# Kernel tuning notes

Measured on AMD Instinct MI355X. Metric: run time of the kernel, lower is better.

## Reference

```python
import jax, jax.numpy as jnp
import numpy as np

B, N = 64, 1024


def setup_inputs() -> dict:
    key = jax.random.key(0)
    attns = jax.random.uniform(key, (B, N, N), dtype=jnp.float32)
    return {"attns": attns}


def _diag_means(a):
    # a: [B, n, n]. wave[b, d] = mean_i a[b, i, i+d] over the anti-diagonal offset d = j - i >= 0.
    n = a.shape[-1]
    idx = jnp.arange(n)
    off = idx[None, :] - idx[:, None]            # [n, n], j - i
    mask = off >= 0                              # upper triangle incl. diagonal
    seg = jnp.where(mask, off, 0).reshape(-1)    # lower-tri values are zeroed, so seg 0 is safe
    vals = jnp.where(mask, a, 0.0).reshape(a.shape[0], -1)  # [B, n*n]
    sums = jax.vmap(lambda v: jax.ops.segment_sum(v, seg, num_segments=n))(vals)  # [B, n]
    counts = (n - idx).astype(a.dtype)           # n - d elements on offset-d diagonal
    return sums / counts


def reference(attns):
    waves = _diag_means(attns)                       # [B, N]
    # torch.fft on (real, 0) pairs + L2 norm over (re, im) == FFT magnitude
    spec = jnp.abs(jnp.fft.fft(waves, axis=-1))      # [B, N]
    n = waves.shape[-1]
    sel = spec[:, 1:1 + n // 2]                      # frequencies 1 .. n/2 (exclusive of DC)
    judgement = 1.0 - jnp.max(sel, axis=-1) / jnp.sum(sel, axis=-1)  # peak-ratio per sample
    return jnp.mean(judgement)                       # scalar, mean over batch
```

## Files before the change

kernel.cpp:

```cpp
#include <hip/hip_runtime.h>

#define NN 1024
#define BB 64
#define CHUNKS 32
#define KS 8

#if __has_builtin(__builtin_amdgcn_make_buffer_rsrc) && __has_builtin(__builtin_amdgcn_raw_buffer_load_b128)
#define USE_SRD 1
#else
#define USE_SRD 0
#endif

#if USE_SRD
typedef unsigned int u32x4 __attribute__((ext_vector_type(4)));
static __device__ __forceinline__ float4 srd_load(__amdgpu_buffer_rsrc_t r, int off) {
    u32x4 v = __builtin_amdgcn_raw_buffer_load_b128(r, off, 0, 0);
    float4 f;
    f.x = __uint_as_float(v.x);
    f.y = __uint_as_float(v.y);
    f.z = __uint_as_float(v.z);
    f.w = __uint_as_float(v.w);
    return f;
}
#endif

__global__ __launch_bounds__(256) void diag_partial(const float* __restrict__ attns,
                                                    float* __restrict__ partial) {
    __shared__ float lds[4][1032];
    const int t = blockIdx.x;
    const int b = blockIdx.y;
    const int tid = threadIdx.x;
    const int w = tid >> 6, lane = tid & 63;

    float4 acc0 = make_float4(0.f, 0.f, 0.f, 0.f);
    float4 acc1 = acc0, acc2 = acc0, acc3 = acc0;

    const float* base = attns + (size_t)b * NN * NN;

#if USE_SRD
    const int voff = lane * 16;

#define ROWPAIR(g, srdT, srdB)                                                \
    const int jbT##g = 16 * t + 4 * (g);                                      \
    const int nvT##g = 256 - 4 * t - (g);                                     \
    __amdgpu_buffer_rsrc_t srdT = __builtin_amdgcn_make_buffer_rsrc(          \
        (void*)(base + (size_t)(jbT##g + w) * NN + jbT##g), (short)0,         \
        nvT##g * 16, 0x00020000);                                             \
    const int jbB##g = 1008 - 16 * t + 4 * (g);                               \
    const int nvB##g = 4 + 4 * t - (g);                                       \
    __amdgpu_buffer_rsrc_t srdB = __builtin_amdgcn_make_buffer_rsrc(          \
        (void*)(base + (size_t)(jbB##g + w) * NN + jbB##g), (short)0,         \
        nvB##g * 16, 0x00020000);

    ROWPAIR(0, srdT0, srdB0)
    ROWPAIR(1, srdT1, srdB1)
    ROWPAIR(2, srdT2, srdB2)
    ROWPAIR(3, srdT3, srdB3)
#undef ROWPAIR

#define LOADP(g, srdT, srdB)                                                  \
    float4 xa##g = srd_load(srdT, voff);                                      \
    float4 xb##g = srd_load(srdT, voff + 1024);                               \
    float4 xc##g = srd_load(srdT, voff + 2048);                               \
    float4 xd##g = srd_load(srdT, voff + 3072);                               \
    float4 ya##g = srd_load(srdB, voff);                                      \
    float4 yb##g = srd_load(srdB, voff + 1024);

#define CONSP(g)                                                              \
    {                                                                         \
        if (lane == 0) {                                                      \
            if (w > 0) { xa##g.x = 0.f; ya##g.x = 0.f; }                      \
            if (w > 1) { xa##g.y = 0.f; ya##g.y = 0.f; }                      \
            if (w > 2) { xa##g.z = 0.f; ya##g.z = 0.f; }                      \
        }                                                                     \
        acc0.x += xa##g.x + ya##g.x; acc0.y += xa##g.y + ya##g.y;             \
        acc0.z += xa##g.z + ya##g.z; acc0.w += xa##g.w + ya##g.w;             \
        acc1.x += xb##g.x + yb##g.x; acc1.y += xb##g.y + yb##g.y;             \
        acc1.z += xb##g.z + yb##g.z; acc1.w += xb##g.w + yb##g.w;             \
        acc2.x += xc##g.x; acc2.y += xc##g.y;                                 \
        acc2.z += xc##g.z; acc2.w += xc##g.w;                                 \
        acc3.x += xd##g.x; acc3.y += xd##g.y;                                 \
        acc3.z += xd##g.z; acc3.w += xd##g.w;                                 \
    }

    LOADP(0, srdT0, srdB0)
    LOADP(1, srdT1, srdB1)
    LOADP(2, srdT2, srdB2)
    CONSP(0)
    LOADP(3, srdT3, srdB3)
    CONSP(1)
    CONSP(2)
    CONSP(3)
#undef LOADP
#undef CONSP

#else

#define ROWPAIR(k, fT, fB, nvT, nvB)                                          \
    const int jbT##k = 16 * t + 4 * (k);                                      \
    const int nvT = 256 - 4 * t - (k);                                        \
    const float4* fT = (const float4*)(base + (size_t)(jbT##k + w) * NN + jbT##k); \
    const int jbB##k = 1008 - 16 * t + 4 * (k);                               \
    const int nvB = 4 + 4 * t - (k);                                          \
    const float4* fB = (const float4*)(base + (size_t)(jbB##k + w) * NN + jbB##k);

    ROWPAIR(0, fT0, fB0, nvT0, nvB0)
    ROWPAIR(1, fT1, fB1, nvT1, nvB1)
    ROWPAIR(2, fT2, fB2, nvT2, nvB2)
    ROWPAIR(3, fT3, fB3, nvT3, nvB3)
#undef ROWPAIR

#define LOADP(g, fT, fB, nvT, nvB)                                            \
    float4 xa##g = fT[lane];                                                  \
    float4 xb##g = fT[lane + 64];                                             \
    float4 xc##g = fT[lane + 128 < nvT - 1 ? lane + 128 : nvT - 1];           \
    float4 xd##g = fT[lane + 192 < nvT - 1 ? lane + 192 : nvT - 1];           \
    float4 ya##g = fB[lane < nvB - 1 ? lane : nvB - 1];                       \
    float4 yb##g = fB[lane + 64 < nvB - 1 ? lane + 64 : nvB - 1];

#define CONSP(g, nvT, nvB)                                                    \
    {                                                                         \
        const bool ok2 = lane + 128 < nvT, ok3 = lane + 192 < nvT;            \
        const bool p0 = lane < nvB, p1 = lane + 64 < nvB;                     \
        xc##g.x = ok2 ? xc##g.x : 0.f; xc##g.y = ok2 ? xc##g.y : 0.f;         \
        xc##g.z = ok2 ? xc##g.z : 0.f; xc##g.w = ok2 ? xc##g.w : 0.f;         \
        xd##g.x = ok3 ? xd##g.x : 0.f; xd##g.y = ok3 ? xd##g.y : 0.f;         \
        xd##g.z = ok3 ? xd##g.z : 0.f; xd##g.w = ok3 ? xd##g.w : 0.f;         \
        ya##g.x = p0 ? ya##g.x : 0.f; ya##g.y = p0 ? ya##g.y : 0.f;           \
        ya##g.z = p0 ? ya##g.z : 0.f; ya##g.w = p0 ? ya##g.w : 0.f;           \
        yb##g.x = p1 ? yb##g.x : 0.f; yb##g.y = p1 ? yb##g.y : 0.f;           \
        yb##g.z = p1 ? yb##g.z : 0.f; yb##g.w = p1 ? yb##g.w : 0.f;           \
        if (lane == 0) {                                                      \
            if (w > 0) { xa##g.x = 0.f; ya##g.x = 0.f; }                      \
            if (w > 1) { xa##g.y = 0.f; ya##g.y = 0.f; }                      \
            if (w > 2) { xa##g.z = 0.f; ya##g.z = 0.f; }                      \
        }                                                                     \
        acc0.x += xa##g.x + ya##g.x; acc0.y += xa##g.y + ya##g.y;             \
        acc0.z += xa##g.z + ya##g.z; acc0.w += xa##g.w + ya##g.w;             \
        acc1.x += xb##g.x + yb##g.x; acc1.y += xb##g.y + yb##g.y;             \
        acc1.z += xb##g.z + yb##g.z; acc1.w += xb##g.w + yb##g.w;             \
        acc2.x += xc##g.x; acc2.y += xc##g.y;                                 \
        acc2.z += xc##g.z; acc2.w += xc##g.w;                                 \
        acc3.x += xd##g.x; acc3.y += xd##g.y;                                 \
        acc3.z += xd##g.z; acc3.w += xd##g.w;                                 \
    }

    LOADP(0, fT0, fB0, nvT0, nvB0)
    LOADP(1, fT1, fB1, nvT1, nvB1)
    LOADP(2, fT2, fB2, nvT2, nvB2)
    CONSP(0, nvT0, nvB0)
    LOADP(3, fT3, fB3, nvT3, nvB3)
    CONSP(1, nvT1, nvB1)
    CONSP(2, nvT2, nvB2)
    CONSP(3, nvT3, nvB3)
#undef LOADP
#undef CONSP
#endif

    float4* lrow = (float4*)lds[w];
    lrow[lane]       = acc0;
    lrow[lane + 64]  = acc1;
    lrow[lane + 128] = acc2;
    lrow[lane + 192] = acc3;
    if (tid < 32) lds[tid >> 3][1024 + (tid & 7)] = 0.f;
    __syncthreads();

    float* outp = partial + ((size_t)b * CHUNKS + t) * NN;
    {
        const int d0 = tid * 4;
        float4 o;
        o.x = (lds[0][d0]     + lds[1][d0 + 1]) + (lds[2][d0 + 2] + lds[3][d0 + 3]);
        o.y = (lds[0][d0 + 1] + lds[1][d0 + 2]) + (lds[2][d0 + 3] + lds[3][d0 + 4]);
        o.z = (lds[0][d0 + 2] + lds[1][d0 + 3]) + (lds[2][d0 + 4] + lds[3][d0 + 5]);
        o.w = (lds[0][d0 + 3] + lds[1][d0 + 4]) + (lds[2][d0 + 5] + lds[3][d0 + 6]);
        ((float4*)outp)[tid] = o;
    }
}

__global__ __launch_bounds__(256) void reduce_waves(const float* __restrict__ partial,
                                                    float* __restrict__ wpm) {
    __shared__ float slo_s[256], shi_s[256];
    const int blk = blockIdx.x;
    const int b = blk >> 3;
    const int dq = blk & 7;
    const int tid = threadIdx.x;
    const int d = dq * 64 + (tid & 63);
    const int cq = tid >> 6;
    const float* pb = partial + (size_t)b * CHUNKS * NN;
    float slo = 0.f, shi = 0.f;
#pragma unroll
    for (int j = 0; j < 8; ++j) {
        const int c = cq * 8 + j;
        slo += pb[c * NN + d];
        shi += pb[c * NN + d + 512];
    }
    slo_s[tid] = slo; shi_s[tid] = shi;
    __syncthreads();
    if (tid < 64) {
        const float l = (slo_s[tid] + slo_s[tid + 64]) + (slo_s[tid + 128] + slo_s[tid + 192]);
        const float h = (shi_s[tid] + shi_s[tid + 64]) + (shi_s[tid + 128] + shi_s[tid + 192]);
        const float wlo = l / (float)(NN - d);
        const float whi = h / (float)(512 - d);
        wpm[(size_t)b * NN + d]       = wlo + whi;
        wpm[(size_t)b * NN + 512 + d] = wlo - whi;
    }
}

__global__ __launch_bounds__(512) void dft_part(const float* __restrict__ wpm,
                                                float* __restrict__ kparts) {
    __shared__ float wp[512], wm[512];
    __shared__ float2 tw[NN];
    __shared__ float redmax[8], redsum[8];
    const int ks = blockIdx.x & (KS - 1);
    const int b = blockIdx.x >> 3;
    const int tid = threadIdx.x;
    const float C = 6.283185307179586f / 1024.0f;

    {
        const float* src = wpm + (size_t)b * NN;
        wp[tid & 511] = src[tid & 511];
        wm[tid & 511] = src[512 + (tid & 511)];
        float s0, c0, s1, c1;
        __sincosf((float)tid * C, &s0, &c0);
        __sincosf((float)(tid + 512) * C, &s1, &c1);
        tw[tid]       = make_float2(c0, -s0);
        tw[tid + 512] = make_float2(c1, -s1);
    }
    __syncthreads();

    const int k = 1 + ks * 64 + (tid >> 3);
    const int dp = tid & 7;
    const float* wsel = (k & 1) ? wm : wp;
    const int kstep = (k << 3) & (NN - 1);

    float re = 0.f, im = 0.f;
    int t = (k * dp) & (NN - 1);
#pragma unroll 8
    for (int it = 0; it < 64; ++it) {
        const float2 c = tw[t];
        const float wv = wsel[dp + 8 * it];
        re = fmaf(wv, c.x, re);
        im = fmaf(wv, c.y, im);
        t = (t + kstep) & (NN - 1);
    }
    re += __shfl_xor(re, 1, 64); re += __shfl_xor(re, 2, 64); re += __shfl_xor(re, 4, 64);
    im += __shfl_xor(im, 1, 64); im += __shfl_xor(im, 2, 64); im += __shfl_xor(im, 4, 64);
    const float spec = sqrtf(re * re + im * im);

    float mx = spec;
    float sm = (dp == 0) ? spec : 0.f;
    for (int off = 8; off < 64; off <<= 1) {
        mx = fmaxf(mx, __shfl_xor(mx, off, 64));
        sm += __shfl_xor(sm, off, 64);
    }
    const int wid = tid >> 6, lane = tid & 63;
    if (lane == 0) { redmax[wid] = mx; redsum[wid] = sm; }
    __syncthreads();
    if (tid == 0) {
        float M = redmax[0], S = redsum[0];
        for (int i = 1; i < 8; ++i) { M = fmaxf(M, redmax[i]); S += redsum[i]; }
        kparts[((size_t)b * KS + ks) * 2 + 0] = M;
        kparts[((size_t)b * KS + ks) * 2 + 1] = S;
    }
}

__global__ __launch_bounds__(64) void finalize(const float* __restrict__ kparts,
                                               float* __restrict__ out) {
    const int lane = threadIdx.x;
    float M = 0.f, S = 0.f;
#pragma unroll
    for (int s = 0; s < KS; ++s) {
        M = fmaxf(M, kparts[((size_t)lane * KS + s) * 2 + 0]);
        S += kparts[((size_t)lane * KS + s) * 2 + 1];
    }
    float j = 1.0f - M / S;
    for (int off = 32; off; off >>= 1) j += __shfl_xor(j, off, 64);
    if (lane == 0) out[0] = j * (1.0f / 64.0f);
}

extern "C" void kernel_launch(void* const* d_in, const int* in_sizes, int n_in,
                              void* d_out, int out_size, void* d_ws, size_t ws_size,
                              hipStream_t stream) {
    const float* attns = (const float*)d_in[0];
    float* out = (float*)d_out;

    float* partial = (float*)d_ws;
    float* wpm     = partial + (size_t)BB * CHUNKS * NN;
    float* kparts  = wpm + (size_t)BB * NN;

    diag_partial<<<dim3(CHUNKS, BB), 256, 0, stream>>>(attns, partial);
    reduce_waves<<<BB * 8, 256, 0, stream>>>(partial, wpm);
    dft_part<<<BB * KS, 512, 0, stream>>>(wpm, kparts);
    finalize<<<1, 64, 0, stream>>>(kparts, out);
}
```

Measured before the change: 39.35 us.

## Cut diagonal partial chunks to 8 with 512-thread blocks covering more row groups

Reduces the number of chunks per batch from 32 to 8. Each diag_partial block now has 8 waves and processes 8 row-pair groups per wave (two quad bodies), with an 8-row LDS combine. This shrinks the partial-sum buffer and the work in reduce_waves, which now sums 8 chunks instead of 32. The trade-off is fewer blocks (512 in total) and longer per-thread work in the main bandwidth-bound pass, which may lower memory-level parallelism.

After: 38.62 us. About the same (-1.8%).

```diff
diff --git a/kernel.cpp b/kernel.cpp
--- a/kernel.cpp
+++ b/kernel.cpp
@@ -2,7 +2,7 @@
 
 #define NN 1024
 #define BB 64
-#define CHUNKS 32
+#define CHUNKS 8
 #define KS 8
 
 #if __has_builtin(__builtin_amdgcn_make_buffer_rsrc) && __has_builtin(__builtin_amdgcn_raw_buffer_load_b128)
@@ -24,13 +24,15 @@
 }
 #endif
 
-__global__ __launch_bounds__(256) void diag_partial(const float* __restrict__ attns,
+__global__ __launch_bounds__(512) void diag_partial(const float* __restrict__ attns,
                                                     float* __restrict__ partial) {
-    __shared__ float lds[4][1032];
+    __shared__ float lds[8][1032];
     const int t = blockIdx.x;
     const int b = blockIdx.y;
     const int tid = threadIdx.x;
     const int w = tid >> 6, lane = tid & 63;
+    const int r = w & 3;
+    const int whi = w >> 2;
 
     float4 acc0 = make_float4(0.f, 0.f, 0.f, 0.f);
     float4 acc1 = acc0, acc2 = acc0, acc3 = acc0;
@@ -40,38 +42,32 @@
 #if USE_SRD
     const int voff = lane * 16;
 
-#define ROWPAIR(g, srdT, srdB)                                                \
-    const int jbT##g = 16 * t + 4 * (g);                                      \
-    const int nvT##g = 256 - 4 * t - (g);                                     \
-    __amdgpu_buffer_rsrc_t srdT = __builtin_amdgcn_make_buffer_rsrc(          \
-        (void*)(base + (size_t)(jbT##g + w) * NN + jbT##g), (short)0,         \
+#define ROWPAIR(g, p)                                                         \
+    const int jbT##g = 64 * t + 8 * (p) + 4 * whi;                            \
+    const int nvT##g = 256 - ((jbT##g) >> 2);                                 \
+    __amdgpu_buffer_rsrc_t srdT##g = __builtin_amdgcn_make_buffer_rsrc(       \
+        (void*)(base + (size_t)(jbT##g + r) * NN + jbT##g), (short)0,         \
         nvT##g * 16, 0x00020000);                                             \
-    const int jbB##g = 1008 - 16 * t + 4 * (g);                               \
-    const int nvB##g = 4 + 4 * t - (g);                                       \
-    __amdgpu_buffer_rsrc_t srdB = __builtin_amdgcn_make_buffer_rsrc(          \
-        (void*)(base + (size_t)(jbB##g + w) * NN + jbB##g), (short)0,         \
+    const int jbB##g = 960 - 64 * t + 8 * (p) + 4 * whi;                      \
+    const int nvB##g = 256 - ((jbB##g) >> 2);                                 \
+    __amdgpu_buffer_rsrc_t srdB##g = __builtin_amdgcn_make_buffer_rsrc(       \
+        (void*)(base + (size_t)(jbB##g + r) * NN + jbB##g), (short)0,         \
         nvB##g * 16, 0x00020000);
 
-    ROWPAIR(0, srdT0, srdB0)
-    ROWPAIR(1, srdT1, srdB1)
-    ROWPAIR(2, srdT2, srdB2)
-    ROWPAIR(3, srdT3, srdB3)
-#undef ROWPAIR
-
-#define LOADP(g, srdT, srdB)                                                  \
-    float4 xa##g = srd_load(srdT, voff);                                      \
-    float4 xb##g = srd_load(srdT, voff + 1024);                               \
-    float4 xc##g = srd_load(srdT, voff + 2048);                               \
-    float4 xd##g = srd_load(srdT, voff + 3072);                               \
-    float4 ya##g = srd_load(srdB, voff);                                      \
-    float4 yb##g = srd_load(srdB, voff + 1024);
+#define LOADP(g)                                                              \
+    float4 xa##g = srd_load(srdT##g, voff);                                   \
+    float4 xb##g = srd_load(srdT##g, voff + 1024);                            \
+    float4 xc##g = srd_load(srdT##g, voff + 2048);                            \
+    float4 xd##g = srd_load(srdT##g, voff + 3072);                            \
+    float4 ya##g = srd_load(srdB##g, voff);                                   \
+    float4 yb##g = srd_load(srdB##g, voff + 1024);
 
 #define CONSP(g)                                                              \
     {                                                                         \
         if (lane == 0) {                                                      \
-            if (w > 0) { xa##g.x = 0.f; ya##g.x = 0.f; }                      \
-            if (w > 1) { xa##g.y = 0.f; ya##g.y = 0.f; }                      \
-            if (w > 2) { xa##g.z = 0.f; ya##g.z = 0.f; }                      \
+            if (r > 0) { xa##g.x = 0.f; ya##g.x = 0.f; }                      \
+            if (r > 1) { xa##g.y = 0.f; ya##g.y = 0.f; }                      \
+            if (r > 2) { xa##g.z = 0.f; ya##g.z = 0.f; }                      \
         }                                                                     \
         acc0.x += xa##g.x + ya##g.x; acc0.y += xa##g.y + ya##g.y;             \
         acc0.z += xa##g.z + ya##g.z; acc0.w += xa##g.w + ya##g.w;             \
@@ -83,45 +79,51 @@
         acc3.z += xd##g.z; acc3.w += xd##g.w;                                 \
     }
 
-    LOADP(0, srdT0, srdB0)
-    LOADP(1, srdT1, srdB1)
-    LOADP(2, srdT2, srdB2)
-    CONSP(0)
-    LOADP(3, srdT3, srdB3)
-    CONSP(1)
-    CONSP(2)
-    CONSP(3)
+#define QUADBODY(P0)                                                          \
+    {                                                                         \
+        ROWPAIR(0, (P0) + 0)                                                  \
+        ROWPAIR(1, (P0) + 1)                                                  \
+        ROWPAIR(2, (P0) + 2)                                                  \
+        ROWPAIR(3, (P0) + 3)                                                  \
+        LOADP(0)                                                              \
+        LOADP(1)                                                              \
+        LOADP(2)                                                              \
+        CONSP(0)                                                              \
+        LOADP(3)                                                              \
+        CONSP(1)                                                              \
+        CONSP(2)                                                              \
+        CONSP(3)                                                              \
+    }
+
+    QUADBODY(0)
+    QUADBODY(4)
+#undef ROWPAIR
 #undef LOADP
 #undef CONSP
+#undef QUADBODY
 
 #else
 
-#define ROWPAIR(k, fT, fB, nvT, nvB)                                          \
-    const int jbT##k = 16 * t + 4 * (k);                                      \
-    const int nvT = 256 - 4 * t - (k);                                        \
-    const float4* fT = (const float4*)(base + (size_t)(jbT##k + w) * NN + jbT##k); \
-    const int jbB##k = 1008 - 16 * t + 4 * (k);                               \
-    const int nvB = 4 + 4 * t - (k);                                          \
-    const float4* fB = (const float4*)(base + (size_t)(jbB##k + w) * NN + jbB##k);
-
-    ROWPAIR(0, fT0, fB0, nvT0, nvB0)
-    ROWPAIR(1, fT1, fB1, nvT1, nvB1)
-    ROWPAIR(2, fT2, fB2, nvT2, nvB2)
-    ROWPAIR(3, fT3, fB3, nvT3, nvB3)
-#undef ROWPAIR
-
-#define LOADP(g, fT, fB, nvT, nvB)                                            \
-    float4 xa##g = fT[lane];                                                  \
-    float4 xb##g = fT[lane + 64];                                             \
-    float4 xc##g = fT[lane + 128 < nvT - 1 ? lane + 128 : nvT - 1];           \
-    float4 xd##g = fT[lane + 192 < nvT - 1 ? lane + 192 : nvT - 1];           \
-    float4 ya##g = fB[lane < nvB - 1 ? lane : nvB - 1];                       \
-    float4 yb##g = fB[lane + 64 < nvB - 1 ? lane + 64 : nvB - 1];
-
-#define CONSP(g, nvT, nvB)                                                    \
+#define ROWPAIR(g, p)                                                         \
+    const int jbT##g = 64 * t + 8 * (p) + 4 * whi;                            \
+    const int nvT##g = 256 - ((jbT##g) >> 2);                                 \
+    const float4* fT##g = (const float4*)(base + (size_t)(jbT##g + r) * NN + jbT##g); \
+    const int jbB##g = 960 - 64 * t + 8 * (p) + 4 * whi;                      \
+    const int nvB##g = 256 - ((jbB##g) >> 2);                                 \
+    const float4* fB##g = (const float4*)(base + (size_t)(jbB##g + r) * NN + jbB##g);
+
+#define LOADP(g)                                                              \
+    float4 xa##g = fT##g[lane];                                               \
+    float4 xb##g = fT##g[lane + 64];                                          \
+    float4 xc##g = fT##g[lane + 128 < nvT##g - 1 ? lane + 128 : nvT##g - 1];  \
+    float4 xd##g = fT##g[lane + 192 < nvT##g - 1 ? lane + 192 : nvT##g - 1];  \
+    float4 ya##g = fB##g[lane < nvB##g - 1 ? lane : nvB##g - 1];              \
+    float4 yb##g = fB##g[lane + 64 < nvB##g - 1 ? lane + 64 : nvB##g - 1];
+
+#define CONSP(g)                                                              \
     {                                                                         \
-        const bool ok2 = lane + 128 < nvT, ok3 = lane + 192 < nvT;            \
-        const bool p0 = lane < nvB, p1 = lane + 64 < nvB;                     \
+        const bool ok2 = lane + 128 < nvT##g, ok3 = lane + 192 < nvT##g;      \
+        const bool p0 = lane < nvB##g, p1 = lane + 64 < nvB##g;               \
         xc##g.x = ok2 ? xc##g.x : 0.f; xc##g.y = ok2 ? xc##g.y : 0.f;         \
         xc##g.z = ok2 ? xc##g.z : 0.f; xc##g.w = ok2 ? xc##g.w : 0.f;         \
         xd##g.x = ok3 ? xd##g.x : 0.f; xd##g.y = ok3 ? xd##g.y : 0.f;         \
@@ -131,9 +133,9 @@
         yb##g.x = p1 ? yb##g.x : 0.f; yb##g.y = p1 ? yb##g.y : 0.f;           \
         yb##g.z = p1 ? yb##g.z : 0.f; yb##g.w = p1 ? yb##g.w : 0.f;           \
         if (lane == 0) {                                                      \
-            if (w > 0) { xa##g.x = 0.f; ya##g.x = 0.f; }                      \
-            if (w > 1) { xa##g.y = 0.f; ya##g.y = 0.f; }                      \
-            if (w > 2) { xa##g.z = 0.f; ya##g.z = 0.f; }                      \
+            if (r > 0) { xa##g.x = 0.f; ya##g.x = 0.f; }                      \
+            if (r > 1) { xa##g.y = 0.f; ya##g.y = 0.f; }                      \
+            if (r > 2) { xa##g.z = 0.f; ya##g.z = 0.f; }                      \
         }                                                                     \
         acc0.x += xa##g.x + ya##g.x; acc0.y += xa##g.y + ya##g.y;             \
         acc0.z += xa##g.z + ya##g.z; acc0.w += xa##g.w + ya##g.w;             \
@@ -145,16 +147,28 @@
         acc3.z += xd##g.z; acc3.w += xd##g.w;                                 \
     }
 
-    LOADP(0, fT0, fB0, nvT0, nvB0)
-    LOADP(1, fT1, fB1, nvT1, nvB1)
-    LOADP(2, fT2, fB2, nvT2, nvB2)
-    CONSP(0, nvT0, nvB0)
-    LOADP(3, fT3, fB3, nvT3, nvB3)
-    CONSP(1, nvT1, nvB1)
-    CONSP(2, nvT2, nvB2)
-    CONSP(3, nvT3, nvB3)
+#define QUADBODY(P0)                                                          \
+    {                                                                         \
+        ROWPAIR(0, (P0) + 0)                                                  \
+        ROWPAIR(1, (P0) + 1)                                                  \
+        ROWPAIR(2, (P0) + 2)                                                  \
+        ROWPAIR(3, (P0) + 3)                                                  \
+        LOADP(0)                                                              \
+        LOADP(1)                                                              \
+        LOADP(2)                                                              \
+        CONSP(0)                                                              \
+        LOADP(3)                                                              \
+        CONSP(1)                                                              \
+        CONSP(2)                                                              \
+        CONSP(3)                                                              \
+    }
+
+    QUADBODY(0)
+    QUADBODY(4)
+#undef ROWPAIR
 #undef LOADP
 #undef CONSP
+#undef QUADBODY
 #endif
 
     float4* lrow = (float4*)lds[w];
@@ -162,18 +176,18 @@
     lrow[lane + 64]  = acc1;
     lrow[lane + 128] = acc2;
     lrow[lane + 192] = acc3;
-    if (tid < 32) lds[tid >> 3][1024 + (tid & 7)] = 0.f;
+    if (tid < 64) lds[tid >> 3][1024 + (tid & 7)] = 0.f;
     __syncthreads();
 
     float* outp = partial + ((size_t)b * CHUNKS + t) * NN;
     {
-        const int d0 = tid * 4;
-        float4 o;
-        o.x = (lds[0][d0]     + lds[1][d0 + 1]) + (lds[2][d0 + 2] + lds[3][d0 + 3]);
-        o.y = (lds[0][d0 + 1] + lds[1][d0 + 2]) + (lds[2][d0 + 3] + lds[3][d0 + 4]);
-        o.z = (lds[0][d0 + 2] + lds[1][d0 + 3]) + (lds[2][d0 + 4] + lds[3][d0 + 5]);
-        o.w = (lds[0][d0 + 3] + lds[1][d0 + 4]) + (lds[2][d0 + 5] + lds[3][d0 + 6]);
-        ((float4*)outp)[tid] = o;
+        const int d0 = tid * 2;
+        float2 o;
+        o.x = ((lds[0][d0]     + lds[1][d0 + 1]) + (lds[2][d0 + 2] + lds[3][d0 + 3]))
+            + ((lds[4][d0]     + lds[5][d0 + 1]) + (lds[6][d0 + 2] + lds[7][d0 + 3]));
+        o.y = ((lds[0][d0 + 1] + lds[1][d0 + 2]) + (lds[2][d0 + 3] + lds[3][d0 + 4]))
+            + ((lds[4][d0 + 1] + lds[5][d0 + 2]) + (lds[6][d0 + 3] + lds[7][d0 + 4]));
+        ((float2*)outp)[tid] = o;
     }
 }
 
@@ -189,8 +203,8 @@
     const float* pb = partial + (size_t)b * CHUNKS * NN;
     float slo = 0.f, shi = 0.f;
 #pragma unroll
-    for (int j = 0; j < 8; ++j) {
-        const int c = cq * 8 + j;
+    for (int j = 0; j < 2; ++j) {
+        const int c = cq * 2 + j;
         slo += pb[c * NN + d];
         shi += pb[c * NN + d + 512];
     }
@@ -288,7 +302,7 @@
     float* wpm     = partial + (size_t)BB * CHUNKS * NN;
     float* kparts  = wpm + (size_t)BB * NN;
 
-    diag_partial<<<dim3(CHUNKS, BB), 256, 0, stream>>>(attns, partial);
+    diag_partial<<<dim3(CHUNKS, BB), 512, 0, stream>>>(attns, partial);
     reduce_waves<<<BB * 8, 256, 0, stream>>>(partial, wpm);
     dft_part<<<BB * KS, 512, 0, stream>>>(wpm, kparts);
     finalize<<<1, 64, 0, stream>>>(kparts, out);
```
